# Performance work log

Hardware: AMD Instinct MI355X
Metric: run time of the kernel (lower is better)

The kernel has to match this reference:

```python
import jax, jax.numpy as jnp
import numpy as np

B, S, NX, H = 8, 1024, 1024, 16
D = NX // H  # head dim = 64


def setup_inputs() -> dict:
    key = jax.random.key(0)
    k1, k2, k3 = jax.random.split(key, 3)
    x = jax.random.normal(k1, (B, S, NX), dtype=jnp.float32)
    Wqkv = jax.random.normal(k2, (NX, 3 * NX), dtype=jnp.float32) * 0.02
    bqkv = jnp.zeros((3 * NX,), dtype=jnp.float32)
    Wproj = jax.random.normal(k3, (NX, NX), dtype=jnp.float32) * 0.02
    bproj = jnp.zeros((NX,), dtype=jnp.float32)
    return {"x": x, "Wqkv": Wqkv, "bqkv": bqkv, "Wproj": Wproj, "bproj": bproj}


def reference(x, Wqkv, bqkv, Wproj, bproj):
    # c_attn: Conv1D == x @ W + b
    qkv = jnp.einsum('bsn,nm->bsm', x, Wqkv) + bqkv  # [B,S,3*NX]
    q, k, v = jnp.split(qkv, 3, axis=-1)
    # split heads -> [B,H,S,D]
    def split_heads(t):
        return t.reshape(B, S, H, D).transpose(0, 2, 1, 3)
    q, k, v = split_heads(q), split_heads(k), split_heads(v)
    # present = stack(key, value) with key as [B,H,S,D]
    present = jnp.stack((k, v))  # [2,B,H,S,D]
    # scores, scaled (scale=True) by sqrt(head_dim)
    w = jnp.einsum('bhqd,bhkd->bhqk', q, k) / jnp.sqrt(jnp.asarray(D, x.dtype))
    bias = jnp.tril(jnp.ones((S, S), dtype=x.dtype))[None, None]  # causal tril buffer
    w = w * bias - 10000.0 * (1.0 - bias)
    w = jax.nn.softmax(w, axis=-1)
    a = jnp.einsum('bhqk,bhkd->bhqd', w, v)  # [B,H,S,D]
    a = a.transpose(0, 2, 1, 3).reshape(B, S, NX)  # merge heads
    a = jnp.einsum('bsn,nm->bsm', a, Wproj) + bproj  # c_proj
    return a, present
```

## Files before the change

### kernel.cpp

```cpp
#include <hip/hip_runtime.h>
#include <stdint.h>


#define BB 8
#define SS 1024
#define NXX 1024
#define NH 16
#define HD 64
#define KK 1024
#define NKT 16

typedef __bf16 bf16x8 __attribute__((ext_vector_type(8)));
typedef float  floatx4 __attribute__((ext_vector_type(4)));
typedef unsigned short ushort8 __attribute__((ext_vector_type(8)));
typedef unsigned short ushortx4 __attribute__((ext_vector_type(4)));

__device__ inline float bf2f(unsigned short u) {
    unsigned int x = ((unsigned int)u) << 16;
    float f;
    __builtin_memcpy(&f, &x, 4);
    return f;
}
__device__ inline unsigned short f2bf(float f) {
    unsigned int u;
    __builtin_memcpy(&u, &f, 4);
    u += 0x7FFFu + ((u >> 16) & 1u);
    return (unsigned short)(u >> 16);
}

__device__ inline void gload_lds16(const unsigned short* g, unsigned short* l) {
    __builtin_amdgcn_global_load_lds(
        (const __attribute__((address_space(1))) void*)g,
        (__attribute__((address_space(3))) void*)l, 16, 0, 0);
}

__device__ inline void barrier_raw() {
    asm volatile("" ::: "memory");
    __builtin_amdgcn_sched_barrier(0);
    __builtin_amdgcn_s_barrier();
    __builtin_amdgcn_sched_barrier(0);
    asm volatile("" ::: "memory");
}
#define WAIT_VM0() asm volatile("s_waitcnt vmcnt(0)" ::: "memory")

__global__ void sniff_k(const unsigned short* __restrict__ x, int* __restrict__ flag) {
    const int lane = threadIdx.x & 63;
    ushort8 v = *(const ushort8*)(x + (size_t)lane * 8);
    int g = 0;
#pragma unroll
    for (int j = 0; j < 8; j++) {
        float f = bf2f(v[j]);
        float a = fabsf(f);
        if (!(a <= 1e4f)) g++;
        else if (f != 0.f && a < 1e-35f) g++;
    }
#pragma unroll
    for (int s = 1; s < 64; s <<= 1) g += __shfl_xor(g, s);
    if (lane == 0 && blockIdx.x == 0) *flag = (g > 16) ? 1 : 0;
}

__global__ __launch_bounds__(256) void prep(
    const void* __restrict__ x, const void* __restrict__ Wqkv,
    const void* __restrict__ Wproj,
    unsigned short* __restrict__ xbf, unsigned short* __restrict__ WqkvT,
    unsigned short* __restrict__ WprojT, const int* __restrict__ flagp) {
    const int f32 = *flagp;
    int blk = blockIdx.x;
    if (blk < 4096) {
        const size_t i = ((size_t)blk * 256 + threadIdx.x) * 8;
        if (f32) {
            const floatx4* p = (const floatx4*)((const float*)x + i);
            floatx4 f0 = p[0], f1 = p[1];
            ushort8 u;
#pragma unroll
            for (int j = 0; j < 4; j++) { u[j] = f2bf(f0[j]); u[4 + j] = f2bf(f1[j]); }
            *(ushort8*)(xbf + i) = u;
        } else {
            *(ushort8*)(xbf + i) = *(const ushort8*)((const unsigned short*)x + i);
        }
        return;
    }
    blk -= 4096;
    const void* in;
    unsigned short* out;
    int R, C;
    if (blk < 3072) { in = Wqkv; out = WqkvT; R = 1024; C = 3072; }
    else            { blk -= 3072; in = Wproj; out = WprojT; R = 1024; C = 1024; }
    const int ctiles = C / 32;
    const int c0 = (blk % ctiles) * 32, r0 = (blk / ctiles) * 32;

    __shared__ unsigned short tile[32][33];
    const int tx = threadIdx.x & 31, ty = threadIdx.x >> 5;
    if (f32) {
        const float* inf = (const float*)in;
#pragma unroll
        for (int i = ty; i < 32; i += 8)
            tile[i][tx] = f2bf(inf[(size_t)(r0 + i) * C + c0 + tx]);
    } else {
        const unsigned short* inu = (const unsigned short*)in;
#pragma unroll
        for (int i = ty; i < 32; i += 8)
            tile[i][tx] = inu[(size_t)(r0 + i) * C + c0 + tx];
    }
    __syncthreads();
#pragma unroll
    for (int i = ty; i < 32; i += 8)
        out[(size_t)(c0 + i) * R + r0 + tx] = tile[tx][i];
}

__global__ __launch_bounds__(256) void transpose_v(
    const void* __restrict__ outbase, unsigned short* __restrict__ vbfT,
    const int* __restrict__ flagp) {
    const int f32 = *flagp;
    const int blk = blockIdx.x;
    const int sb = blk & 15;
    const int bh = blk >> 4;
    const int tid = threadIdx.x;
    const int r = tid >> 2;
    const int c0 = (tid & 3) * 16;
    __shared__ unsigned short tile[64][72];
    const int perm = ((r & 15) << 2) | (r >> 4);
    const size_t esz = f32 ? 4 : 2;
    const char* vbase = (const char*)outbase + (size_t)(2 * BB * SS * NXX) * esz;
    if (f32) {
        const float* src = (const float*)vbase + ((size_t)bh * SS + sb * 64 + r) * HD + c0;
#pragma unroll
        for (int j = 0; j < 16; j++) tile[c0 + j][perm] = f2bf(src[j]);
    } else {
        const unsigned short* src = (const unsigned short*)vbase + ((size_t)bh * SS + sb * 64 + r) * HD + c0;
#pragma unroll
        for (int j = 0; j < 16; j++) tile[c0 + j][perm] = src[j];
    }
    __syncthreads();
    const int d = tid >> 2;
    const int o0 = (tid & 3) * 16;
    unsigned short* dst = vbfT + ((size_t)(bh * HD + d)) * SS + sb * 64 + o0;
    *(ushort8*)dst       = *(const ushort8*)&tile[d][o0];
    *(ushort8*)(dst + 8) = *(const ushort8*)&tile[d][o0 + 8];
}

#define STAGE_A(slot, h, kt) do { \
    const unsigned short* sg_ = Ab + (size_t)((h) * 128) * KK + (size_t)(kt) * 64; \
    gload_lds16(sg_, &As[slot][(h) * 8192 + w * 512]); \
    gload_lds16(sg_ + (size_t)64 * KK, &As[slot][(h) * 8192 + 4096 + w * 512]); \
} while (0)
#define STAGE_B(slot, j, kt) do { \
    const unsigned short* sg_ = Bb + (size_t)((j) * 64) * KK + (size_t)(kt) * 64; \
    gload_lds16(sg_, &Bs[slot][(j) * 4096 + w * 512]); \
} while (0)
#define LOADA(dst, qq) do { \
    _Pragma("unroll") \
    for (int mm = 0; mm < 2; mm++) { \
        const int arow = (qq) * 32 + mm * 16 + l15; \
        dst[mm][0] = *(const bf16x8*)&Ah[arow * 64 + fo0]; \
        dst[mm][1] = *(const bf16x8*)&Ah[arow * 64 + fo1]; \
    } \
} while (0)
#define MFMAQ(qq, ar) do { \
    __builtin_amdgcn_s_setprio(1); \
    _Pragma("unroll") \
    for (int mm = 0; mm < 2; mm++) \
    _Pragma("unroll") \
    for (int nf = 0; nf < NF; nf++) { \
        acc[2 * (qq) + mm][nf] = __builtin_amdgcn_mfma_f32_16x16x32_bf16(ar[mm][0], bfr[nf][0], acc[2 * (qq) + mm][nf], 0, 0, 0); \
        acc[2 * (qq) + mm][nf] = __builtin_amdgcn_mfma_f32_16x16x32_bf16(ar[mm][1], bfr[nf][1], acc[2 * (qq) + mm][nf], 0, 0, 0); \
    } \
    __builtin_amdgcn_s_setprio(0); \
} while (0)
#define WAIT_VMNF() do { \
    if constexpr (NF == 2)      asm volatile("s_waitcnt vmcnt(2)" ::: "memory"); \
    else if constexpr (NF == 3) asm volatile("s_waitcnt vmcnt(3)" ::: "memory"); \
    else                        asm volatile("s_waitcnt vmcnt(4)" ::: "memory"); \
} while (0)

template <int MODE, int NF>
__global__ __launch_bounds__(512, 2) void gemm8p(
    const unsigned short* __restrict__ A,
    const unsigned short* __restrict__ Bt,
    const void* __restrict__ bias,
    void* __restrict__ outbase,
    unsigned short* __restrict__ q_ws,
    unsigned short* __restrict__ kbf,
    int N, int Nt, const int* __restrict__ flagp) {
    __shared__ __align__(16) unsigned short As[2][2 * 8192];
    __shared__ __align__(16) unsigned short Bs[2][NF * 4096];

    const int f32 = *flagp;
    const int tid  = threadIdx.x;
    const int lane = tid & 63;
    const int w = tid >> 6;
    const int r = w >> 2;
    const int c = w & 3;
    const int l15 = lane & 15;
    const int quad = lane >> 4;

    const int cpx = gridDim.x >> 3;
    const int bid = (blockIdx.x & 7) * cpx + (blockIdx.x >> 3);
    const int bx = bid % Nt, by = bid / Nt;
    const int row0 = by * 256, col0 = bx * (64 * NF);

    floatx4 acc[8][NF];
    floatx4 zz = {0.f, 0.f, 0.f, 0.f};
#pragma unroll
    for (int i = 0; i < 8; i++)
#pragma unroll
        for (int j = 0; j < NF; j++) acc[i][j] = zz;

    const int srow = tid >> 3;
    const int scole = ((tid & 7) ^ (srow & 7)) << 3;
    const unsigned short* Ab = A  + (size_t)(row0 + srow) * KK + scole;
    const unsigned short* Bb = Bt + (size_t)(col0 + srow) * KK + scole;

    const int fo0 = (quad << 3) ^ ((l15 & 7) << 3);
    const int fo1 = fo0 ^ 32;

    STAGE_A(0, 0, 0); STAGE_A(0, 1, 0);
#pragma unroll
    for (int j = 0; j < NF; j++) STAGE_B(0, j, 0);
#pragma unroll
    for (int j = 0; j < NF; j++) STAGE_B(1, j, 1);
    WAIT_VMNF();
    barrier_raw();

    bf16x8 bfr[NF][2], aX[2][2], aY[2][2];
#pragma unroll 2
    for (int t = 0; t < NKT; t++) {
        const int slot = t & 1;
        const unsigned short* Ah = &As[slot][r * 8192];
        const unsigned short* Bh = &Bs[slot][0];
#pragma unroll
        for (int nf = 0; nf < NF; nf++) {
            const int brow = c * (16 * NF) + nf * 16 + l15;
            bfr[nf][0] = *(const bf16x8*)&Bh[brow * 64 + fo0];
            bfr[nf][1] = *(const bf16x8*)&Bh[brow * 64 + fo1];
        }
        LOADA(aX, 0);
        LOADA(aY, 1);
        if (t + 1 < NKT) STAGE_A(slot ^ 1, 0, t + 1);
        barrier_raw();
        MFMAQ(0, aX);
        barrier_raw();
        LOADA(aX, 2);
        if (t + 1 < NKT) STAGE_A(slot ^ 1, 1, t + 1);
        barrier_raw();
        MFMAQ(1, aY);
        barrier_raw();
        LOADA(aY, 3);
        if (t + 2 < NKT) {
#pragma unroll
            for (int j = 0; j < (NF + 1) / 2; j++) STAGE_B(slot, j, t + 2);
        }
        barrier_raw();
        MFMAQ(2, aX);
        barrier_raw();
        if (t + 2 < NKT) {
#pragma unroll
            for (int j = (NF + 1) / 2; j < NF; j++) STAGE_B(slot, j, t + 2);
        }
        barrier_raw();
        MFMAQ(3, aY);
        if (t < NKT - 2) { WAIT_VMNF(); } else { WAIT_VM0(); }
        barrier_raw();
    }

    float bv[NF];
#pragma unroll
    for (int nf = 0; nf < NF; nf++) {
        const int colb = col0 + c * (16 * NF) + nf * 16 + l15;
        bv[nf] = f32 ? ((const float*)bias)[colb] : bf2f(((const unsigned short*)bias)[colb]);
    }

    if (MODE == 0) {
#pragma unroll
        for (int nf = 0; nf < NF; nf++) {
            const int colb = col0 + c * (16 * NF) + nf * 16 + l15;
#pragma unroll
            for (int mi = 0; mi < 8; mi++)
#pragma unroll
                for (int i = 0; i < 4; i++) {
                    const int row = row0 + r * 128 + mi * 16 + quad * 4 + i;
                    const float val = acc[mi][nf][i] + bv[nf];
                    const size_t idx = (size_t)row * N + colb;
                    if (f32) ((float*)outbase)[idx] = val;
                    else     ((unsigned short*)outbase)[idx] = f2bf(val);
                }
        }
        return;
    }

    const size_t esz = f32 ? 4 : 2;
    const int b = row0 >> 10;
    const int s0 = row0 & 1023;

#pragma unroll
    for (int nf = 0; nf < NF; nf++) {
        const int colb = col0 + c * (16 * NF) + nf * 16 + l15;
        const int sec = colb >> 10;
        const int h = (colb & 1023) >> 6, d = colb & 63;
        if (sec == 0) {
#pragma unroll
            for (int mi = 0; mi < 8; mi++)
#pragma unroll
                for (int i = 0; i < 4; i++) {
                    const int s = s0 + r * 128 + mi * 16 + quad * 4 + i;
                    q_ws[(size_t)((b * NH + h) * SS + s) * HD + d] = f2bf(acc[mi][nf][i] + bv[nf]);
                }
        } else if (sec == 1) {
            char* kbase = (char*)outbase + (size_t)(BB * SS * NXX) * esz;
#pragma unroll
            for (int mi = 0; mi < 8; mi++)
#pragma unroll
                for (int i = 0; i < 4; i++) {
                    const int s = s0 + r * 128 + mi * 16 + quad * 4 + i;
                    const float val = acc[mi][nf][i] + bv[nf];
                    const size_t idx = (size_t)((b * NH + h) * SS + s) * HD + d;
                    if (f32) ((float*)kbase)[idx] = val;
                    else     ((unsigned short*)kbase)[idx] = f2bf(val);
                    kbf[idx] = f2bf(val);
                }
        } else {
            char* vbase = (char*)outbase + (size_t)(2 * BB * SS * NXX) * esz;
#pragma unroll
            for (int mi = 0; mi < 8; mi++)
#pragma unroll
                for (int i = 0; i < 4; i++) {
                    const int s = s0 + r * 128 + mi * 16 + quad * 4 + i;
                    const float val = acc[mi][nf][i] + bv[nf];
                    const size_t idx = (size_t)((b * NH + h) * SS + s) * HD + d;
                    if (f32) ((float*)vbase)[idx] = val;
                    else     ((unsigned short*)vbase)[idx] = f2bf(val);
                }
        }
    }
}

__global__ __launch_bounds__(256) void attn(
    const unsigned short* __restrict__ q_ws,
    const unsigned short* __restrict__ kbf,
    const unsigned short* __restrict__ vbfT,
    unsigned short* __restrict__ amerged) {
    const int tid = threadIdx.x;
    const int lane = tid & 63;
    const int w = tid >> 6;
    const int l15 = lane & 15, quad = lane >> 4;
    const int blk = blockIdx.x;
    const int p = blk & 3;
    const int bh = blk >> 2;
    const int b = bh >> 4, h = bh & 15;

    const unsigned short* Q = q_ws + (size_t)bh * (SS * HD);
    const unsigned short* K = kbf + (size_t)bh * (SS * HD);
    const unsigned short* V = vbfT + (size_t)bh * (HD * SS);

    __shared__ __align__(16) unsigned short Ks[64][72];
    __shared__ __align__(16) unsigned short Vs[64][72];
    __shared__ __align__(16) unsigned short Pl[4][32][72];

    floatx4 zz = {0.f, 0.f, 0.f, 0.f};
    ushort8 ones_u;
#pragma unroll
    for (int j = 0; j < 8; j++) ones_u[j] = 0x3F80;
    const bf16x8 ones = __builtin_bit_cast(bf16x8, ones_u);

    const int srow = tid >> 2;
    const int soff = (tid & 3) * 16;

#pragma unroll
    for (int tile = 0; tile < 2; tile++) {
        const int qb = tile ? (7 - p) : p;
        const int qbase = qb * 128;
        const int wrow0 = qbase + w * 32;
        const int wq_max = wrow0 + 31;
        const int jend = qbase + 128;

        bf16x8 qa[2][2];
#pragma unroll
        for (int m = 0; m < 2; m++)
#pragma unroll
            for (int t = 0; t < 2; t++)
                qa[m][t] = *(const bf16x8*)&Q[(size_t)(wrow0 + m * 16 + l15) * HD + t * 32 + quad * 8];

        floatx4 o[2][4], o5[2];
        float mrow[2][4];
#pragma unroll
        for (int m = 0; m < 2; m++) {
            o5[m] = zz;
#pragma unroll
            for (int i = 0; i < 4; i++) mrow[m][i] = -1e30f;
#pragma unroll
            for (int nf = 0; nf < 4; nf++) o[m][nf] = zz;
        }

        *(ushort8*)&Ks[srow][soff]     = *(const ushort8*)&K[(size_t)srow * HD + soff];
        *(ushort8*)&Ks[srow][soff + 8] = *(const ushort8*)&K[(size_t)srow * HD + soff + 8];
        *(ushort8*)&Vs[srow][soff]     = *(const ushort8*)&V[(size_t)srow * SS + soff];
        *(ushort8*)&Vs[srow][soff + 8] = *(const ushort8*)&V[(size_t)srow * SS + soff + 8];
        __syncthreads();

        for (int j0 = 0; j0 < jend; j0 += 64) {
            const bool havenext = (j0 + 64 < jend);
            ushort8 kn0, kn1, vn0, vn1;
            if (havenext) {
                kn0 = *(const ushort8*)&K[(size_t)(j0 + 64 + srow) * HD + soff];
                kn1 = *(const ushort8*)&K[(size_t)(j0 + 64 + srow) * HD + soff + 8];
                vn0 = *(const ushort8*)&V[(size_t)srow * SS + j0 + 64 + soff];
                vn1 = *(const ushort8*)&V[(size_t)srow * SS + j0 + 64 + soff + 8];
            }

            if (j0 <= wq_max) {
                floatx4 sf[2][4];
#pragma unroll
                for (int kg = 0; kg < 4; kg++) {
                    bf16x8 kb0 = *(const bf16x8*)&Ks[kg * 16 + l15][quad * 8];
                    bf16x8 kb1 = *(const bf16x8*)&Ks[kg * 16 + l15][32 + quad * 8];
#pragma unroll
                    for (int m = 0; m < 2; m++) {
                        floatx4 s = zz;
                        s = __builtin_amdgcn_mfma_f32_16x16x32_bf16(qa[m][0], kb0, s, 0, 0, 0);
                        s = __builtin_amdgcn_mfma_f32_16x16x32_bf16(qa[m][1], kb1, s, 0, 0, 0);
                        sf[m][kg] = s;
                    }
                }

                float alpha_[2][4];
#pragma unroll
                for (int m = 0; m < 2; m++)
#pragma unroll
                    for (int i = 0; i < 4; i++) {
                        const int qrow = wrow0 + m * 16 + quad * 4 + i;
                        float pv4[4];
#pragma unroll
                        for (int kg = 0; kg < 4; kg++) {
                            const int key = j0 + kg * 16 + l15;
                            float s = sf[m][kg][i] * 0.125f;
                            if (key > qrow) s = -10000.0f;
                            pv4[kg] = s;
                        }
                        float t = fmaxf(fmaxf(pv4[0], pv4[1]), fmaxf(pv4[2], pv4[3]));
                        t = fmaxf(t, __shfl_xor(t, 1));
                        t = fmaxf(t, __shfl_xor(t, 2));
                        t = fmaxf(t, __shfl_xor(t, 4));
                        t = fmaxf(t, __shfl_xor(t, 8));
                        const float mnew = fmaxf(mrow[m][i], t);
                        alpha_[m][i] = __expf(mrow[m][i] - mnew);
                        mrow[m][i] = mnew;
                        ushortx4 pk;
#pragma unroll
                        for (int kg = 0; kg < 4; kg++)
                            pk[kg] = f2bf(__expf(pv4[kg] - mnew));
                        *(ushortx4*)&Pl[w][m * 16 + quad * 4 + i][l15 * 4] = pk;
                    }

#pragma unroll
                for (int m = 0; m < 2; m++) {
#pragma unroll
                    for (int i = 0; i < 4; i++) o5[m][i] *= alpha_[m][i];
#pragma unroll
                    for (int nf = 0; nf < 4; nf++)
#pragma unroll
                        for (int i = 0; i < 4; i++) o[m][nf][i] *= alpha_[m][i];
                }

                bf16x8 pa[2][2];
#pragma unroll
                for (int m = 0; m < 2; m++) {
                    pa[m][0] = *(const bf16x8*)&Pl[w][m * 16 + l15][quad * 8];
                    pa[m][1] = *(const bf16x8*)&Pl[w][m * 16 + l15][32 + quad * 8];
                }

#pragma unroll
                for (int m = 0; m < 2; m++) {
                    o5[m] = __builtin_amdgcn_mfma_f32_16x16x32_bf16(pa[m][0], ones, o5[m], 0, 0, 0);
                    o5[m] = __builtin_amdgcn_mfma_f32_16x16x32_bf16(pa[m][1], ones, o5[m], 0, 0, 0);
                }
#pragma unroll
                for (int nf = 0; nf < 4; nf++) {
                    bf16x8 vb0 = *(const bf16x8*)&Vs[nf * 16 + l15][quad * 8];
                    bf16x8 vb1 = *(const bf16x8*)&Vs[nf * 16 + l15][32 + quad * 8];
#pragma unroll
                    for (int m = 0; m < 2; m++) {
                        o[m][nf] = __builtin_amdgcn_mfma_f32_16x16x32_bf16(pa[m][0], vb0, o[m][nf], 0, 0, 0);
                        o[m][nf] = __builtin_amdgcn_mfma_f32_16x16x32_bf16(pa[m][1], vb1, o[m][nf], 0, 0, 0);
                    }
                }
            }
            __syncthreads();
            if (havenext) {
                *(ushort8*)&Ks[srow][soff]     = kn0;
                *(ushort8*)&Ks[srow][soff + 8] = kn1;
                *(ushort8*)&Vs[srow][soff]     = vn0;
                *(ushort8*)&Vs[srow][soff + 8] = vn1;
            }
            __syncthreads();
        }

#pragma unroll
        for (int m = 0; m < 2; m++)
#pragma unroll
            for (int nf = 0; nf < 4; nf++)
#pragma unroll
                for (int i = 0; i < 4; i++) {
                    const int s = wrow0 + m * 16 + quad * 4 + i;
                    amerged[(size_t)(b * SS + s) * NXX + h * HD + nf * 16 + l15] =
                        f2bf(o[m][nf][i] / o5[m][i]);
                }
        __syncthreads();
    }
}

extern "C" void kernel_launch(void* const* d_in, const int* in_sizes, int n_in,
                              void* d_out, int out_size, void* d_ws, size_t ws_size,
                              hipStream_t stream) {
    const void* x     = d_in[0];
    const void* Wqkv  = d_in[1];
    const void* bqkv  = d_in[2];
    const void* Wproj = d_in[3];
    const void* bproj = d_in[4];

    int* flag = (int*)d_ws;
    unsigned short* ws = (unsigned short*)d_ws + 8;
    unsigned short* WqkvT   = ws;
    unsigned short* WprojT  = WqkvT + 3072 * 1024;
    unsigned short* q_ws    = WprojT + 1024 * 1024;
    unsigned short* kbf     = q_ws + 8 * 1024 * 1024;
    unsigned short* vbfT    = kbf + 8 * 1024 * 1024;
    unsigned short* amerged = vbfT + 8 * 1024 * 1024;
    unsigned short* xbf     = amerged;

    sniff_k<<<1, 64, 0, stream>>>((const unsigned short*)x, flag);
    prep<<<dim3(8192), 256, 0, stream>>>(x, Wqkv, Wproj, xbf, WqkvT, WprojT, flag);
    gemm8p<1, 3><<<dim3(512), 512, 0, stream>>>(
        xbf, WqkvT, bqkv, d_out, q_ws, kbf, 3072, 16, flag);
    transpose_v<<<dim3(128 * 16), 256, 0, stream>>>(d_out, vbfT, flag);
    attn<<<dim3(BB * NH * 4), 256, 0, stream>>>(q_ws, kbf, vbfT, amerged);
    gemm8p<0, 2><<<dim3(256), 512, 0, stream>>>(
        amerged, WprojT, bproj, d_out, nullptr, nullptr, 1024, 8, flag);
}
```

Baseline: 326.1 us.

## Fuse V transpose into QKV GEMM epilogue and split attention into one tile per block

The separate transpose_v kernel is removed. The QKV GEMM epilogue now stages its output tile in shared memory (reusing the A/B staging pool) and writes Q, K and present with coalesced 16-byte stores, and writes the transposed, permuted V directly. The attention kernel drops the paired-tile loop (p and 7-p) and launches 8 query blocks per head, one tile each, with launch_bounds(256,4). This removes a kernel launch and the extra round trip of V through global memory, at the cost of causal load imbalance across blocks and an extra LDS pass and barrier in the GEMM epilogue.

```diff
diff --git a/kernel.cpp b/kernel.cpp
--- a/kernel.cpp
+++ b/kernel.cpp
@@ -108,45 +108,16 @@
         out[(size_t)(c0 + i) * R + r0 + tx] = tile[tx][i];
 }
 
-__global__ __launch_bounds__(256) void transpose_v(
-    const void* __restrict__ outbase, unsigned short* __restrict__ vbfT,
-    const int* __restrict__ flagp) {
-    const int f32 = *flagp;
-    const int blk = blockIdx.x;
-    const int sb = blk & 15;
-    const int bh = blk >> 4;
-    const int tid = threadIdx.x;
-    const int r = tid >> 2;
-    const int c0 = (tid & 3) * 16;
-    __shared__ unsigned short tile[64][72];
-    const int perm = ((r & 15) << 2) | (r >> 4);
-    const size_t esz = f32 ? 4 : 2;
-    const char* vbase = (const char*)outbase + (size_t)(2 * BB * SS * NXX) * esz;
-    if (f32) {
-        const float* src = (const float*)vbase + ((size_t)bh * SS + sb * 64 + r) * HD + c0;
-#pragma unroll
-        for (int j = 0; j < 16; j++) tile[c0 + j][perm] = f2bf(src[j]);
-    } else {
-        const unsigned short* src = (const unsigned short*)vbase + ((size_t)bh * SS + sb * 64 + r) * HD + c0;
-#pragma unroll
-        for (int j = 0; j < 16; j++) tile[c0 + j][perm] = src[j];
-    }
-    __syncthreads();
-    const int d = tid >> 2;
-    const int o0 = (tid & 3) * 16;
-    unsigned short* dst = vbfT + ((size_t)(bh * HD + d)) * SS + sb * 64 + o0;
-    *(ushort8*)dst       = *(const ushort8*)&tile[d][o0];
-    *(ushort8*)(dst + 8) = *(const ushort8*)&tile[d][o0 + 8];
-}
-
+#define ASOFF(slot) ((slot) * 16384)
+#define BSOFF(slot) (32768 + (slot) * NF * 4096)
 #define STAGE_A(slot, h, kt) do { \
     const unsigned short* sg_ = Ab + (size_t)((h) * 128) * KK + (size_t)(kt) * 64; \
-    gload_lds16(sg_, &As[slot][(h) * 8192 + w * 512]); \
-    gload_lds16(sg_ + (size_t)64 * KK, &As[slot][(h) * 8192 + 4096 + w * 512]); \
+    gload_lds16(sg_, &POOL[ASOFF(slot) + (h) * 8192 + w * 512]); \
+    gload_lds16(sg_ + (size_t)64 * KK, &POOL[ASOFF(slot) + (h) * 8192 + 4096 + w * 512]); \
 } while (0)
 #define STAGE_B(slot, j, kt) do { \
     const unsigned short* sg_ = Bb + (size_t)((j) * 64) * KK + (size_t)(kt) * 64; \
-    gload_lds16(sg_, &Bs[slot][(j) * 4096 + w * 512]); \
+    gload_lds16(sg_, &POOL[BSOFF(slot) + (j) * 4096 + w * 512]); \
 } while (0)
 #define LOADA(dst, qq) do { \
     _Pragma("unroll") \
@@ -181,9 +152,10 @@
     void* __restrict__ outbase,
     unsigned short* __restrict__ q_ws,
     unsigned short* __restrict__ kbf,
+    unsigned short* __restrict__ vbfT,
     int N, int Nt, const int* __restrict__ flagp) {
-    __shared__ __align__(16) unsigned short As[2][2 * 8192];
-    __shared__ __align__(16) unsigned short Bs[2][NF * 4096];
+    __shared__ __align__(16) unsigned short POOL[2 * 2 * 8192 + 2 * NF * 4096];
+    constexpr int TBW = 64 * NF + 12;
 
     const int f32 = *flagp;
     const int tid  = threadIdx.x;
@@ -226,8 +198,8 @@
 #pragma unroll 2
     for (int t = 0; t < NKT; t++) {
         const int slot = t & 1;
-        const unsigned short* Ah = &As[slot][r * 8192];
-        const unsigned short* Bh = &Bs[slot][0];
+        const unsigned short* Ah = &POOL[ASOFF(slot) + r * 8192];
+        const unsigned short* Bh = &POOL[BSOFF(slot)];
 #pragma unroll
         for (int nf = 0; nf < NF; nf++) {
             const int brow = c * (16 * NF) + nf * 16 + l15;
@@ -288,53 +260,70 @@
         return;
     }
 
-    const size_t esz = f32 ? 4 : 2;
-    const int b = row0 >> 10;
-    const int s0 = row0 & 1023;
-
-#pragma unroll
-    for (int nf = 0; nf < NF; nf++) {
-        const int colb = col0 + c * (16 * NF) + nf * 16 + l15;
-        const int sec = colb >> 10;
-        const int h = (colb & 1023) >> 6, d = colb & 63;
-        if (sec == 0) {
+    if constexpr (MODE == 1) {
+        const size_t esz = f32 ? 4 : 2;
+        const int b = row0 >> 10;
+        const int s0 = row0 & 1023;
+        unsigned short* TB = POOL;
+
+#pragma unroll
+        for (int nf = 0; nf < NF; nf++) {
+            const int colc = c * (16 * NF) + nf * 16 + l15;
+            const int colb = col0 + colc;
+            const int sec = colb >> 10;
+            const int h = (colb & 1023) >> 6, d = colb & 63;
 #pragma unroll
             for (int mi = 0; mi < 8; mi++)
 #pragma unroll
                 for (int i = 0; i < 4; i++) {
-                    const int s = s0 + r * 128 + mi * 16 + quad * 4 + i;
-                    q_ws[(size_t)((b * NH + h) * SS + s) * HD + d] = f2bf(acc[mi][nf][i] + bv[nf]);
+                    const int sl = r * 128 + mi * 16 + quad * 4 + i;
+                    const float val = acc[mi][nf][i] + bv[nf];
+                    TB[sl * TBW + colc] = f2bf(val);
+                    if (f32) {
+                        const size_t idx = (size_t)((b * NH + h) * SS + s0 + sl) * HD + d;
+                        if (sec == 1)      ((float*)((char*)outbase + (size_t)(BB * SS * NXX) * esz))[idx] = val;
+                        else if (sec == 2) ((float*)((char*)outbase + (size_t)(2 * BB * SS * NXX) * esz))[idx] = val;
+                    }
                 }
-        } else if (sec == 1) {
-            char* kbase = (char*)outbase + (size_t)(BB * SS * NXX) * esz;
-#pragma unroll
-            for (int mi = 0; mi < 8; mi++)
-#pragma unroll
-                for (int i = 0; i < 4; i++) {
-                    const int s = s0 + r * 128 + mi * 16 + quad * 4 + i;
-                    const float val = acc[mi][nf][i] + bv[nf];
-                    const size_t idx = (size_t)((b * NH + h) * SS + s) * HD + d;
-                    if (f32) ((float*)kbase)[idx] = val;
-                    else     ((unsigned short*)kbase)[idx] = f2bf(val);
-                    kbf[idx] = f2bf(val);
-                }
-        } else {
-            char* vbase = (char*)outbase + (size_t)(2 * BB * SS * NXX) * esz;
-#pragma unroll
-            for (int mi = 0; mi < 8; mi++)
-#pragma unroll
-                for (int i = 0; i < 4; i++) {
-                    const int s = s0 + r * 128 + mi * 16 + quad * 4 + i;
-                    const float val = acc[mi][nf][i] + bv[nf];
-                    const size_t idx = (size_t)((b * NH + h) * SS + s) * HD + d;
-                    if (f32) ((float*)vbase)[idx] = val;
-                    else     ((unsigned short*)vbase)[idx] = f2bf(val);
-                }
-        }
-    }
-}
-
-__global__ __launch_bounds__(256) void attn(
+        }
+        __syncthreads();
+
+        for (int rg = tid; rg < 256 * NF * 8; rg += 512) {
+            const int c8 = (rg % (NF * 8)) * 8;
+            const int s  = rg / (NF * 8);
+            const int colb = col0 + c8;
+            const int sec = colb >> 10;
+            const int h = (colb & 1023) >> 6, d0 = colb & 63;
+            const size_t dstoff = (size_t)((b * NH + h) * SS + s0 + s) * HD + d0;
+            ushort8 v8 = *(const ushort8*)&TB[s * TBW + c8];
+            if (sec == 0) {
+                *(ushort8*)(q_ws + dstoff) = v8;
+            } else if (sec == 1) {
+                *(ushort8*)(kbf + dstoff) = v8;
+                if (!f32) *(ushort8*)((unsigned short*)outbase + (size_t)(BB * SS * NXX) + dstoff) = v8;
+            } else {
+                if (!f32) *(ushort8*)((unsigned short*)outbase + (size_t)(2 * BB * SS * NXX) + dstoff) = v8;
+            }
+        }
+        for (int rg = tid; rg < NF * 64 * 32; rg += 512) {
+            const int col = rg >> 5;
+            const int colb = col0 + col;
+            if ((colb >> 10) != 2) continue;
+            const int orun = (rg & 31) * 8;
+            const int h = (colb & 1023) >> 6, d = colb & 63;
+            ushort8 v8;
+#pragma unroll
+            for (int k2 = 0; k2 < 8; k2++) {
+                const int o = orun + k2;
+                const int sl = (o & ~63) + (((o & 3) << 4) | ((o & 63) >> 2));
+                v8[k2] = TB[sl * TBW + col];
+            }
+            *(ushort8*)&vbfT[(size_t)((b * NH + h) * HD + d) * SS + s0 + orun] = v8;
+        }
+    }
+}
+
+__global__ __launch_bounds__(256, 4) void attn(
     const unsigned short* __restrict__ q_ws,
     const unsigned short* __restrict__ kbf,
     const unsigned short* __restrict__ vbfT,
@@ -344,8 +333,8 @@
     const int w = tid >> 6;
     const int l15 = lane & 15, quad = lane >> 4;
     const int blk = blockIdx.x;
-    const int p = blk & 3;
-    const int bh = blk >> 2;
+    const int qb = blk & 7;
+    const int bh = blk >> 3;
     const int b = bh >> 4, h = bh & 15;
 
     const unsigned short* Q = q_ws + (size_t)bh * (SS * HD);
@@ -365,147 +354,142 @@
     const int srow = tid >> 2;
     const int soff = (tid & 3) * 16;
 
-#pragma unroll
-    for (int tile = 0; tile < 2; tile++) {
-        const int qb = tile ? (7 - p) : p;
-        const int qbase = qb * 128;
-        const int wrow0 = qbase + w * 32;
-        const int wq_max = wrow0 + 31;
-        const int jend = qbase + 128;
-
-        bf16x8 qa[2][2];
-#pragma unroll
-        for (int m = 0; m < 2; m++)
-#pragma unroll
-            for (int t = 0; t < 2; t++)
-                qa[m][t] = *(const bf16x8*)&Q[(size_t)(wrow0 + m * 16 + l15) * HD + t * 32 + quad * 8];
-
-        floatx4 o[2][4], o5[2];
-        float mrow[2][4];
-#pragma unroll
-        for (int m = 0; m < 2; m++) {
-            o5[m] = zz;
-#pragma unroll
-            for (int i = 0; i < 4; i++) mrow[m][i] = -1e30f;
-#pragma unroll
-            for (int nf = 0; nf < 4; nf++) o[m][nf] = zz;
-        }
-
-        *(ushort8*)&Ks[srow][soff]     = *(const ushort8*)&K[(size_t)srow * HD + soff];
-        *(ushort8*)&Ks[srow][soff + 8] = *(const ushort8*)&K[(size_t)srow * HD + soff + 8];
-        *(ushort8*)&Vs[srow][soff]     = *(const ushort8*)&V[(size_t)srow * SS + soff];
-        *(ushort8*)&Vs[srow][soff + 8] = *(const ushort8*)&V[(size_t)srow * SS + soff + 8];
+    const int qbase = qb * 128;
+    const int wrow0 = qbase + w * 32;
+    const int wq_max = wrow0 + 31;
+    const int jend = qbase + 128;
+
+    bf16x8 qa[2][2];
+#pragma unroll
+    for (int m = 0; m < 2; m++)
+#pragma unroll
+        for (int t = 0; t < 2; t++)
+            qa[m][t] = *(const bf16x8*)&Q[(size_t)(wrow0 + m * 16 + l15) * HD + t * 32 + quad * 8];
+
+    floatx4 o[2][4], o5[2];
+    float mrow[2][4];
+#pragma unroll
+    for (int m = 0; m < 2; m++) {
+        o5[m] = zz;
+#pragma unroll
+        for (int i = 0; i < 4; i++) mrow[m][i] = -1e30f;
+#pragma unroll
+        for (int nf = 0; nf < 4; nf++) o[m][nf] = zz;
+    }
+
+    *(ushort8*)&Ks[srow][soff]     = *(const ushort8*)&K[(size_t)srow * HD + soff];
+    *(ushort8*)&Ks[srow][soff + 8] = *(const ushort8*)&K[(size_t)srow * HD + soff + 8];
+    *(ushort8*)&Vs[srow][soff]     = *(const ushort8*)&V[(size_t)srow * SS + soff];
+    *(ushort8*)&Vs[srow][soff + 8] = *(const ushort8*)&V[(size_t)srow * SS + soff + 8];
+    __syncthreads();
+
+    for (int j0 = 0; j0 < jend; j0 += 64) {
+        const bool havenext = (j0 + 64 < jend);
+        ushort8 kn0, kn1, vn0, vn1;
+        if (havenext) {
+            kn0 = *(const ushort8*)&K[(size_t)(j0 + 64 + srow) * HD + soff];
+            kn1 = *(const ushort8*)&K[(size_t)(j0 + 64 + srow) * HD + soff + 8];
+            vn0 = *(const ushort8*)&V[(size_t)srow * SS + j0 + 64 + soff];
+            vn1 = *(const ushort8*)&V[(size_t)srow * SS + j0 + 64 + soff + 8];
+        }
+
+        if (j0 <= wq_max) {
+            floatx4 sf[2][4];
+#pragma unroll
+            for (int kg = 0; kg < 4; kg++) {
+                bf16x8 kb0 = *(const bf16x8*)&Ks[kg * 16 + l15][quad * 8];
+                bf16x8 kb1 = *(const bf16x8*)&Ks[kg * 16 + l15][32 + quad * 8];
+#pragma unroll
+                for (int m = 0; m < 2; m++) {
+                    floatx4 s = zz;
+                    s = __builtin_amdgcn_mfma_f32_16x16x32_bf16(qa[m][0], kb0, s, 0, 0, 0);
+                    s = __builtin_amdgcn_mfma_f32_16x16x32_bf16(qa[m][1], kb1, s, 0, 0, 0);
+                    sf[m][kg] = s;
+                }
+            }
+
+            float alpha_[2][4];
+#pragma unroll
+            for (int m = 0; m < 2; m++)
+#pragma unroll
+                for (int i = 0; i < 4; i++) {
+                    const int qrow = wrow0 + m * 16 + quad * 4 + i;
+                    float pv4[4];
+#pragma unroll
+                    for (int kg = 0; kg < 4; kg++) {
+                        const int key = j0 + kg * 16 + l15;
+                        float s = sf[m][kg][i] * 0.125f;
+                        if (key > qrow) s = -10000.0f;
+                        pv4[kg] = s;
+                    }
+                    float t = fmaxf(fmaxf(pv4[0], pv4[1]), fmaxf(pv4[2], pv4[3]));
+                    t = fmaxf(t, __shfl_xor(t, 1));
+                    t = fmaxf(t, __shfl_xor(t, 2));
+                    t = fmaxf(t, __shfl_xor(t, 4));
+                    t = fmaxf(t, __shfl_xor(t, 8));
+                    const float mnew = fmaxf(mrow[m][i], t);
+                    alpha_[m][i] = __expf(mrow[m][i] - mnew);
+                    mrow[m][i] = mnew;
+                    ushortx4 pk;
+#pragma unroll
+                    for (int kg = 0; kg < 4; kg++)
+                        pk[kg] = f2bf(__expf(pv4[kg] - mnew));
+                    *(ushortx4*)&Pl[w][m * 16 + quad * 4 + i][l15 * 4] = pk;
+                }
+
+#pragma unroll
+            for (int m = 0; m < 2; m++) {
+#pragma unroll
+                for (int i = 0; i < 4; i++) o5[m][i] *= alpha_[m][i];
+#pragma unroll
+                for (int nf = 0; nf < 4; nf++)
+#pragma unroll
+                    for (int i = 0; i < 4; i++) o[m][nf][i] *= alpha_[m][i];
+            }
+
+            bf16x8 pa[2][2];
+#pragma unroll
+            for (int m = 0; m < 2; m++) {
+                pa[m][0] = *(const bf16x8*)&Pl[w][m * 16 + l15][quad * 8];
+                pa[m][1] = *(const bf16x8*)&Pl[w][m * 16 + l15][32 + quad * 8];
+            }
+
+#pragma unroll
+            for (int m = 0; m < 2; m++) {
+                o5[m] = __builtin_amdgcn_mfma_f32_16x16x32_bf16(pa[m][0], ones, o5[m], 0, 0, 0);
+                o5[m] = __builtin_amdgcn_mfma_f32_16x16x32_bf16(pa[m][1], ones, o5[m], 0, 0, 0);
+            }
+#pragma unroll
+            for (int nf = 0; nf < 4; nf++) {
+                bf16x8 vb0 = *(const bf16x8*)&Vs[nf * 16 + l15][quad * 8];
+                bf16x8 vb1 = *(const bf16x8*)&Vs[nf * 16 + l15][32 + quad * 8];
+#pragma unroll
+                for (int m = 0; m < 2; m++) {
+                    o[m][nf] = __builtin_amdgcn_mfma_f32_16x16x32_bf16(pa[m][0], vb0, o[m][nf], 0, 0, 0);
+                    o[m][nf] = __builtin_amdgcn_mfma_f32_16x16x32_bf16(pa[m][1], vb1, o[m][nf], 0, 0, 0);
+                }
+            }
+        }
         __syncthreads();
-
-        for (int j0 = 0; j0 < jend; j0 += 64) {
-            const bool havenext = (j0 + 64 < jend);
-            ushort8 kn0, kn1, vn0, vn1;
-            if (havenext) {
-                kn0 = *(const ushort8*)&K[(size_t)(j0 + 64 + srow) * HD + soff];
-                kn1 = *(const ushort8*)&K[(size_t)(j0 + 64 + srow) * HD + soff + 8];
-                vn0 = *(const ushort8*)&V[(size_t)srow * SS + j0 + 64 + soff];
-                vn1 = *(const ushort8*)&V[(size_t)srow * SS + j0 + 64 + soff + 8];
-            }
-
-            if (j0 <= wq_max) {
-                floatx4 sf[2][4];
-#pragma unroll
-                for (int kg = 0; kg < 4; kg++) {
-                    bf16x8 kb0 = *(const bf16x8*)&Ks[kg * 16 + l15][quad * 8];
-                    bf16x8 kb1 = *(const bf16x8*)&Ks[kg * 16 + l15][32 + quad * 8];
-#pragma unroll
-                    for (int m = 0; m < 2; m++) {
-                        floatx4 s = zz;
-                        s = __builtin_amdgcn_mfma_f32_16x16x32_bf16(qa[m][0], kb0, s, 0, 0, 0);
-                        s = __builtin_amdgcn_mfma_f32_16x16x32_bf16(qa[m][1], kb1, s, 0, 0, 0);
-                        sf[m][kg] = s;
-                    }
-                }
-
-                float alpha_[2][4];
-#pragma unroll
-                for (int m = 0; m < 2; m++)
-#pragma unroll
-                    for (int i = 0; i < 4; i++) {
-                        const int qrow = wrow0 + m * 16 + quad * 4 + i;
-                        float pv4[4];
-#pragma unroll
-                        for (int kg = 0; kg < 4; kg++) {
-                            const int key = j0 + kg * 16 + l15;
-                            float s = sf[m][kg][i] * 0.125f;
-                            if (key > qrow) s = -10000.0f;
-                            pv4[kg] = s;
-                        }
-                        float t = fmaxf(fmaxf(pv4[0], pv4[1]), fmaxf(pv4[2], pv4[3]));
-                        t = fmaxf(t, __shfl_xor(t, 1));
-                        t = fmaxf(t, __shfl_xor(t, 2));
-                        t = fmaxf(t, __shfl_xor(t, 4));
-                        t = fmaxf(t, __shfl_xor(t, 8));
-                        const float mnew = fmaxf(mrow[m][i], t);
-                        alpha_[m][i] = __expf(mrow[m][i] - mnew);
-                        mrow[m][i] = mnew;
-                        ushortx4 pk;
-#pragma unroll
-                        for (int kg = 0; kg < 4; kg++)
-                            pk[kg] = f2bf(__expf(pv4[kg] - mnew));
-                        *(ushortx4*)&Pl[w][m * 16 + quad * 4 + i][l15 * 4] = pk;
-                    }
-
-#pragma unroll
-                for (int m = 0; m < 2; m++) {
-#pragma unroll
-                    for (int i = 0; i < 4; i++) o5[m][i] *= alpha_[m][i];
-#pragma unroll
-                    for (int nf = 0; nf < 4; nf++)
-#pragma unroll
-                        for (int i = 0; i < 4; i++) o[m][nf][i] *= alpha_[m][i];
-                }
-
-                bf16x8 pa[2][2];
-#pragma unroll
-                for (int m = 0; m < 2; m++) {
-                    pa[m][0] = *(const bf16x8*)&Pl[w][m * 16 + l15][quad * 8];
-                    pa[m][1] = *(const bf16x8*)&Pl[w][m * 16 + l15][32 + quad * 8];
-                }
-
-#pragma unroll
-                for (int m = 0; m < 2; m++) {
-                    o5[m] = __builtin_amdgcn_mfma_f32_16x16x32_bf16(pa[m][0], ones, o5[m], 0, 0, 0);
-                    o5[m] = __builtin_amdgcn_mfma_f32_16x16x32_bf16(pa[m][1], ones, o5[m], 0, 0, 0);
-                }
-#pragma unroll
-                for (int nf = 0; nf < 4; nf++) {
-                    bf16x8 vb0 = *(const bf16x8*)&Vs[nf * 16 + l15][quad * 8];
-                    bf16x8 vb1 = *(const bf16x8*)&Vs[nf * 16 + l15][32 + quad * 8];
-#pragma unroll
-                    for (int m = 0; m < 2; m++) {
-                        o[m][nf] = __builtin_amdgcn_mfma_f32_16x16x32_bf16(pa[m][0], vb0, o[m][nf], 0, 0, 0);
-                        o[m][nf] = __builtin_amdgcn_mfma_f32_16x16x32_bf16(pa[m][1], vb1, o[m][nf], 0, 0, 0);
-                    }
-                }
-            }
-            __syncthreads();
-            if (havenext) {
-                *(ushort8*)&Ks[srow][soff]     = kn0;
-                *(ushort8*)&Ks[srow][soff + 8] = kn1;
-                *(ushort8*)&Vs[srow][soff]     = vn0;
-                *(ushort8*)&Vs[srow][soff + 8] = vn1;
-            }
-            __syncthreads();
-        }
-
-#pragma unroll
-        for (int m = 0; m < 2; m++)
-#pragma unroll
-            for (int nf = 0; nf < 4; nf++)
-#pragma unroll
-                for (int i = 0; i < 4; i++) {
-                    const int s = wrow0 + m * 16 + quad * 4 + i;
-                    amerged[(size_t)(b * SS + s) * NXX + h * HD + nf * 16 + l15] =
-                        f2bf(o[m][nf][i] / o5[m][i]);
-                }
+        if (havenext) {
+            *(ushort8*)&Ks[srow][soff]     = kn0;
+            *(ushort8*)&Ks[srow][soff + 8] = kn1;
+            *(ushort8*)&Vs[srow][soff]     = vn0;
+            *(ushort8*)&Vs[srow][soff + 8] = vn1;
+        }
         __syncthreads();
     }
+
+#pragma unroll
+    for (int m = 0; m < 2; m++)
+#pragma unroll
+        for (int nf = 0; nf < 4; nf++)
+#pragma unroll
+            for (int i = 0; i < 4; i++) {
+                const int s = wrow0 + m * 16 + quad * 4 + i;
+                amerged[(size_t)(b * SS + s) * NXX + h * HD + nf * 16 + l15] =
+                    f2bf(o[m][nf][i] / o5[m][i]);
+            }
 }
 
 extern "C" void kernel_launch(void* const* d_in, const int* in_sizes, int n_in,
@@ -530,9 +514,8 @@
     sniff_k<<<1, 64, 0, stream>>>((const unsigned short*)x, flag);
     prep<<<dim3(8192), 256, 0, stream>>>(x, Wqkv, Wproj, xbf, WqkvT, WprojT, flag);
     gemm8p<1, 3><<<dim3(512), 512, 0, stream>>>(
-        xbf, WqkvT, bqkv, d_out, q_ws, kbf, 3072, 16, flag);
-    transpose_v<<<dim3(128 * 16), 256, 0, stream>>>(d_out, vbfT, flag);
-    attn<<<dim3(BB * NH * 4), 256, 0, stream>>>(q_ws, kbf, vbfT, amerged);
+        xbf, WqkvT, bqkv, d_out, q_ws, kbf, vbfT, 3072, 16, flag);
+    attn<<<dim3(BB * NH * 8), 256, 0, stream>>>(q_ws, kbf, vbfT, amerged);
     gemm8p<0, 2><<<dim3(256), 512, 0, stream>>>(
-        amerged, WprojT, bproj, d_out, nullptr, nullptr, 1024, 8, flag);
-}
+        amerged, WprojT, bproj, d_out, nullptr, nullptr, nullptr, 1024, 8, flag);
+}
```

Result: slower. 348.8 us (+7.0%).
